# Performance work log

Hardware: AMD Instinct MI355X
Metric: run time of the kernel (lower is better)

Reference implementation:

```python
import jax, jax.numpy as jnp
import numpy as np


def _graph_conv_mean(x, src, dst, edge_weight, W_rel, W_root, b, num_nodes):
    # messages: gather source features, optionally scale by edge weight
    msg = x[src]  # [E, D]
    if edge_weight is not None:
        msg = msg * edge_weight[:, None]
    # mean aggregation over incoming edges per destination node
    summed = jax.ops.segment_sum(msg, dst, num_segments=num_nodes)  # [N, D]
    count = jax.ops.segment_sum(jnp.ones((src.shape[0],), x.dtype), dst, num_segments=num_nodes)
    mean = summed / jnp.maximum(count, 1.0)[:, None]
    # out = lin_rel(mean) + lin_root(x) + bias
    return mean @ W_rel + x @ W_root + b


def setup_inputs() -> dict:
    key = jax.random.key(0)
    ks = jax.random.split(key, 8)
    N, E, D, H, C = 100000, 1600000, 128, 32, 5
    x = jax.random.normal(ks[0], (N, D), dtype=jnp.float32)
    edge_index = jax.random.randint(ks[1], (2, E), 0, N, dtype=jnp.int64)
    edge_weight = jax.random.uniform(ks[2], (E,), dtype=jnp.float32)
    W_rel1 = jax.random.normal(ks[3], (D, H), dtype=jnp.float32) / np.sqrt(D)
    W_root1 = jax.random.normal(ks[4], (D, H), dtype=jnp.float32) / np.sqrt(D)
    b1 = jnp.zeros((H,), jnp.float32)
    W_rel2 = jax.random.normal(ks[5], (H, C), dtype=jnp.float32) / np.sqrt(H)
    W_root2 = jax.random.normal(ks[6], (H, C), dtype=jnp.float32) / np.sqrt(H)
    b2 = jnp.zeros((C,), jnp.float32)
    return {"x": x, "edge_index": edge_index, "edge_weight": edge_weight,
            "W_rel1": W_rel1, "W_root1": W_root1, "b1": b1,
            "W_rel2": W_rel2, "W_root2": W_root2, "b2": b2}


def reference(x, edge_index, edge_weight, W_rel1, W_root1, b1, W_rel2, W_root2, b2):
    N = x.shape[0]
    src, dst = edge_index[0], edge_index[1]
    # conv1 with edge_weight
    h = _graph_conv_mean(x, src, dst, edge_weight, W_rel1, W_root1, b1, N)
    h = jax.nn.relu(h)
    # dropout is identity at inference (training=False)
    # conv2 without edge_weight
    out = _graph_conv_mean(h, src, dst, None, W_rel2, W_root2, b2, N)
    return jax.nn.log_softmax(out, axis=1)
```

## Files before the change

kernel.cpp:

```cpp
#include <hip/hip_runtime.h>
#include <math.h>

#define N_NODES 100000
#define E_EDGES 1600000
#define D_IN    128
#define H_MID   32
#define C_OUT   5

#define BSHIFT 8
#define BNODES 256
#define NBKT   391
#define BCAP   4800
#define SRC_BITS 17
#define SRC_MASK 0x1FFFF

#define KP 136

typedef __attribute__((ext_vector_type(8))) short bf16x8;
typedef __attribute__((ext_vector_type(4))) float f32x4;

__device__ inline unsigned f2bf(float f) {
    unsigned u = __float_as_uint(f);
    return (u + 0x7FFFu + ((u >> 16) & 1u)) >> 16;
}

__global__ void k_prep(const float* __restrict__ Wrel,
                       const float* __restrict__ Wroot,
                       int* __restrict__ bucket_cursor,
                       unsigned short* __restrict__ wt_g) {
    int tid = threadIdx.x;
    bucket_cursor[tid] = 0;
    for (int i = tid; i < 64 * 128; i += 512) {
        int n = i >> 7, k = i & 127;
        float v = (n < H_MID) ? Wrel[k * H_MID + n] : Wroot[k * H_MID + (n - H_MID)];
        wt_g[i] = (unsigned short)f2bf(v);
    }
}

__global__ __launch_bounds__(256) void k1_mfma(
    const float* __restrict__ x,
    const unsigned short* __restrict__ wt_g,
    const float* __restrict__ b1,
    unsigned short* __restrict__ xrelh,
    float* __restrict__ xroot) {
    __shared__ unsigned short xs[64 * KP];
    int tid = threadIdx.x;
    int nodeBase = blockIdx.x * 64;

    #pragma unroll
    for (int it = 0; it < 16; ++it) {
        int idx = it * 256 + tid;
        int row = idx >> 6, kp = idx & 63;
        int node = nodeBase + row;
        float2 v = make_float2(0.f, 0.f);
        if (node < N_NODES)
            v = *(const float2*)(x + (size_t)node * D_IN + kp * 2);
        unsigned pk = f2bf(v.x) | (f2bf(v.y) << 16);
        *(unsigned*)(xs + row * KP + kp * 2) = pk;
    }
    __syncthreads();

    int lane = tid & 63;
    int wv = tid >> 6;
    int m = lane & 15;
    int quad = lane >> 4;

    f32x4 acc[4];
    #pragma unroll
    for (int nt = 0; nt < 4; ++nt) acc[nt] = (f32x4){0.f, 0.f, 0.f, 0.f};

    #pragma unroll
    for (int kk = 0; kk < 4; ++kk) {
        int k0 = kk * 32 + quad * 8;
        bf16x8 a = *(const bf16x8*)(xs + (wv * 16 + m) * KP + k0);
        #pragma unroll
        for (int nt = 0; nt < 4; ++nt) {
            bf16x8 b = *(const bf16x8*)(wt_g + (nt * 16 + m) * 128 + k0);
            acc[nt] = __builtin_amdgcn_mfma_f32_16x16x32_bf16(a, b, acc[nt], 0, 0, 0);
        }
    }

    #pragma unroll
    for (int nt = 0; nt < 4; ++nt) {
        #pragma unroll
        for (int r = 0; r < 4; ++r) {
            int node = nodeBase + wv * 16 + quad * 4 + r;
            int colg = nt * 16 + m;
            if (node < N_NODES) {
                if (colg < H_MID) {
                    xrelh[(size_t)node * H_MID + colg] =
                        (unsigned short)f2bf(acc[nt][r]);
                } else {
                    int c = colg - H_MID;
                    xroot[(size_t)node * H_MID + c] = acc[nt][r] + b1[c];
                }
            }
        }
    }
}

__global__ __launch_bounds__(1024) void k_binA(
    const int* __restrict__ src,
    const int* __restrict__ dst,
    const float* __restrict__ ew,
    int* __restrict__ bucket_cursor,
    int2* __restrict__ staged) {
    __shared__ int cnt[NBKT];
    __shared__ int lstart[NBKT];
    __shared__ int gbase[NBKT];
    __shared__ int scanbuf[512];
    __shared__ int2 ebuf[2048];
    __shared__ short bbuf[2048];
    int tid = threadIdx.x;
    int eBase = blockIdx.x * 2048;

    if (tid < NBKT) cnt[tid] = 0;
    __syncthreads();

    int b[2], rank[2], packed[2], wbits[2];
    bool valid[2];
    #pragma unroll
    for (int u = 0; u < 2; ++u) {
        int e = eBase + u * 1024 + tid;
        valid[u] = (e < E_EDGES);
        b[u] = 0; rank[u] = 0; packed[u] = 0; wbits[u] = 0;
        if (valid[u]) {
            int d = dst[e];
            int s = src[e];
            wbits[u] = __float_as_int(ew[e]);
            b[u] = d >> BSHIFT;
            packed[u] = ((d & (BNODES - 1)) << SRC_BITS) | s;
            rank[u] = atomicAdd(&cnt[b[u]], 1);
        }
    }
    __syncthreads();

    if (tid < 512) scanbuf[tid] = (tid < NBKT) ? cnt[tid] : 0;
    __syncthreads();
    for (int off = 1; off < 512; off <<= 1) {
        int t = 0;
        if (tid < 512 && tid >= off) t = scanbuf[tid - off];
        __syncthreads();
        if (tid < 512) scanbuf[tid] += t;
        __syncthreads();
    }
    if (tid < NBKT) {
        lstart[tid] = scanbuf[tid] - cnt[tid];
        gbase[tid]  = atomicAdd(&bucket_cursor[tid], cnt[tid]);
    }
    __syncthreads();
    int total = scanbuf[NBKT - 1];

    #pragma unroll
    for (int u = 0; u < 2; ++u) {
        if (valid[u]) {
            int slot = lstart[b[u]] + rank[u];
            ebuf[slot] = make_int2(packed[u], wbits[u]);
            bbuf[slot] = (short)b[u];
        }
    }
    __syncthreads();

    for (int t = tid; t < total; t += 1024) {
        int2 ev = ebuf[t];
        int bb = bbuf[t];
        int gpos = gbase[bb] + (t - lstart[bb]);
        if (gpos < BCAP)
            staged[(size_t)bb * BCAP + gpos] = ev;
    }
}

__global__ __launch_bounds__(1024) void k_binB2(
    const int* __restrict__ bucket_cursor,
    const int2* __restrict__ staged,
    int* __restrict__ deg,
    int* __restrict__ offsets,
    int* __restrict__ csr_src,
    int* __restrict__ csr_wi) {
    __shared__ int hist[BNODES];
    __shared__ int scanb[BNODES];
    __shared__ int cur[BNODES];
    __shared__ int sbase[512];
    int tid = threadIdx.x;
    int b = blockIdx.x;

    if (tid < 512) {
        int c = (tid < NBKT) ? bucket_cursor[tid] : 0;
        sbase[tid] = (c > BCAP) ? BCAP : c;
    }
    if (tid < BNODES) hist[tid] = 0;
    __syncthreads();
    for (int off = 1; off < 512; off <<= 1) {
        int t = 0;
        if (tid < 512 && tid >= off) t = sbase[tid - off];
        __syncthreads();
        if (tid < 512) sbase[tid] += t;
        __syncthreads();
    }
    int count = bucket_cursor[b];
    if (count > BCAP) count = BCAP;
    int base = sbase[b] - count;
    int nodeBase = b << BSHIFT;
    const int2* sp = staged + (size_t)b * BCAP;

    for (int i = tid; i < count; i += 1024)
        atomicAdd(&hist[((unsigned)sp[i].x) >> SRC_BITS], 1);
    __syncthreads();

    int v = 0;
    if (tid < BNODES) {
        v = hist[tid];
        scanb[tid] = v;
    }
    __syncthreads();
    for (int off = 1; off < BNODES; off <<= 1) {
        int t = 0;
        if (tid < BNODES && tid >= off) t = scanb[tid - off];
        __syncthreads();
        if (tid < BNODES) scanb[tid] += t;
        __syncthreads();
    }
    if (tid < BNODES) {
        int excl = scanb[tid] - v;
        int node = nodeBase + tid;
        if (node < N_NODES) {
            deg[node]     = v;
            offsets[node] = base + excl;
        }
        cur[tid] = excl;
    }
    __syncthreads();

    for (int i = tid; i < count; i += 1024) {
        int2 ev = sp[i];
        int local = ((unsigned)ev.x) >> SRC_BITS;
        int pos = base + atomicAdd(&cur[local], 1);
        csr_src[pos] = ev.x & SRC_MASK;
        csr_wi[pos]  = ev.y;
    }
}

__global__ __launch_bounds__(256) void k_layer1(
    const int* __restrict__ offsets,
    const int* __restrict__ deg,
    const int* __restrict__ csr_src,
    const float* __restrict__ csr_w,
    const unsigned short* __restrict__ xrelh,
    const float* __restrict__ xroot,
    const float* __restrict__ Wrel2,
    const float* __restrict__ Wroot2,
    const float* __restrict__ b2,
    float* __restrict__ h2rel,
    float* __restrict__ h2root) {
    int node = blockIdx.x * 16 + (threadIdx.x >> 4);
    int lane = threadIdx.x & 15;
    int beg = offsets[node];
    int dg  = deg[node];
    int end = beg + dg;

    float acc0 = 0.f, acc1 = 0.f;
    int i = beg;
    int nfull = dg >> 3;
    if (nfull) {
        int s[8]; float w[8];
        #pragma unroll
        for (int u = 0; u < 8; ++u) { s[u] = csr_src[i + u]; w[u] = csr_w[i + u]; }
        for (int bb = 1; bb < nfull; ++bb) {
            unsigned v[8];
            #pragma unroll
            for (int u = 0; u < 8; ++u)
                v[u] = *(const unsigned*)(xrelh + (size_t)s[u] * H_MID + lane * 2);
            int s2[8]; float w2[8];
            #pragma unroll
            for (int u = 0; u < 8; ++u) { s2[u] = csr_src[i + 8 + u]; w2[u] = csr_w[i + 8 + u]; }
            #pragma unroll
            for (int u = 0; u < 8; ++u) {
                acc0 += __uint_as_float((v[u] & 0xFFFFu) << 16) * w[u];
                acc1 += __uint_as_float(v[u] & 0xFFFF0000u) * w[u];
            }
            #pragma unroll
            for (int u = 0; u < 8; ++u) { s[u] = s2[u]; w[u] = w2[u]; }
            i += 8;
        }
        unsigned v[8];
        #pragma unroll
        for (int u = 0; u < 8; ++u)
            v[u] = *(const unsigned*)(xrelh + (size_t)s[u] * H_MID + lane * 2);
        #pragma unroll
        for (int u = 0; u < 8; ++u) {
            acc0 += __uint_as_float((v[u] & 0xFFFFu) << 16) * w[u];
            acc1 += __uint_as_float(v[u] & 0xFFFF0000u) * w[u];
        }
        i += 8;
    }
    for (; i < end; ++i) {
        int s0 = csr_src[i];
        float w0 = csr_w[i];
        unsigned v0 = *(const unsigned*)(xrelh + (size_t)s0 * H_MID + lane * 2);
        acc0 += __uint_as_float((v0 & 0xFFFFu) << 16) * w0;
        acc1 += __uint_as_float(v0 & 0xFFFF0000u) * w0;
    }

    float inv = 1.0f / fmaxf((float)dg, 1.0f);
    float2 rt = *(const float2*)(xroot + (size_t)node * H_MID + lane * 2);
    float h0 = fmaxf(acc0 * inv + rt.x, 0.f);
    float h1 = fmaxf(acc1 * inv + rt.y, 0.f);

    float p[2 * C_OUT];
    #pragma unroll
    for (int j = 0; j < C_OUT; ++j) {
        p[j]         = h0 * Wrel2[(2 * lane) * C_OUT + j]
                     + h1 * Wrel2[(2 * lane + 1) * C_OUT + j];
        p[C_OUT + j] = h0 * Wroot2[(2 * lane) * C_OUT + j]
                     + h1 * Wroot2[(2 * lane + 1) * C_OUT + j];
    }
    #pragma unroll
    for (int mm = 8; mm > 0; mm >>= 1) {
        #pragma unroll
        for (int j = 0; j < 2 * C_OUT; ++j)
            p[j] += __shfl_xor(p[j], mm, 16);
    }
    if (lane == 0) {
        #pragma unroll
        for (int j = 0; j < C_OUT; ++j) {
            h2rel[(size_t)node * C_OUT + j]  = p[j];
            h2root[(size_t)node * C_OUT + j] = p[C_OUT + j] + b2[j];
        }
    }
}

__global__ __launch_bounds__(256) void k_layer2(
    const int* __restrict__ offsets,
    const int* __restrict__ deg,
    const int* __restrict__ csr_src,
    const float* __restrict__ h2rel,
    const float* __restrict__ h2root,
    float* __restrict__ out) {
    int node = blockIdx.x * 32 + (threadIdx.x >> 3);
    int lane = threadIdx.x & 7;
    int beg = offsets[node];
    int dg  = deg[node];
    int end = beg + dg;

    float acc = 0.f;
    if (lane < C_OUT) {
        int i = beg;
        int nfull = dg >> 3;
        if (nfull) {
            int s[8];
            #pragma unroll
            for (int u = 0; u < 8; ++u) s[u] = csr_src[i + u];
            for (int bb = 1; bb < nfull; ++bb) {
                float v[8];
                #pragma unroll
                for (int u = 0; u < 8; ++u)
                    v[u] = h2rel[(size_t)s[u] * C_OUT + lane];
                int s2[8];
                #pragma unroll
                for (int u = 0; u < 8; ++u) s2[u] = csr_src[i + 8 + u];
                #pragma unroll
                for (int u = 0; u < 8; ++u) acc += v[u];
                #pragma unroll
                for (int u = 0; u < 8; ++u) s[u] = s2[u];
                i += 8;
            }
            #pragma unroll
            for (int u = 0; u < 8; ++u)
                acc += h2rel[(size_t)s[u] * C_OUT + lane];
            i += 8;
        }
        for (; i < end; ++i)
            acc += h2rel[(size_t)csr_src[i] * C_OUT + lane];
    }
    float inv = 1.0f / fmaxf((float)dg, 1.0f);
    float o = (lane < C_OUT)
                  ? acc * inv + h2root[(size_t)node * C_OUT + lane]
                  : -INFINITY;
    float m = o;
    #pragma unroll
    for (int dd = 4; dd > 0; dd >>= 1) m = fmaxf(m, __shfl_xor(m, dd, 8));
    float e = (lane < C_OUT) ? expf(o - m) : 0.f;
    float ssum = e;
    #pragma unroll
    for (int dd = 4; dd > 0; dd >>= 1) ssum += __shfl_xor(ssum, dd, 8);
    float lse = m + logf(ssum);
    if (lane < C_OUT)
        out[(size_t)node * C_OUT + lane] = o - lse;
}

extern "C" void kernel_launch(void* const* d_in, const int* in_sizes, int n_in,
                              void* d_out, int out_size, void* d_ws, size_t ws_size,
                              hipStream_t stream) {
    const float* x      = (const float*)d_in[0];
    const int*   ei     = (const int*)d_in[1];
    const float* ew     = (const float*)d_in[2];
    const float* Wrel1  = (const float*)d_in[3];
    const float* Wroot1 = (const float*)d_in[4];
    const float* b1     = (const float*)d_in[5];
    const float* Wrel2  = (const float*)d_in[6];
    const float* Wroot2 = (const float*)d_in[7];
    const float* b2     = (const float*)d_in[8];
    float* out = (float*)d_out;

    const int* src = ei;
    const int* dst = ei + E_EDGES;

    char* ws = (char*)d_ws;
    int*   deg           = (int*)ws;
    int*   bucket_cursor = deg + N_NODES;
    unsigned short* wt_g = (unsigned short*)(bucket_cursor + 512);
    int*   offsets       = (int*)(wt_g + 64 * 128);
    int*   csr_src       = offsets + N_NODES;
    int*   csr_wi        = csr_src + E_EDGES;
    unsigned short* xrelh = (unsigned short*)(csr_wi + E_EDGES);
    float* xroot         = (float*)(xrelh + (size_t)N_NODES * H_MID);
    float* h2rel         = xroot + (size_t)N_NODES * H_MID;
    float* h2root        = h2rel + (size_t)N_NODES * C_OUT;
    int2*  staged        = (int2*)xrelh;

    k_prep<<<1, 512, 0, stream>>>(Wrel1, Wroot1, bucket_cursor, wt_g);

    k_binA<<<(E_EDGES + 2047) / 2048, 1024, 0, stream>>>(src, dst, ew,
                                                         bucket_cursor, staged);
    k_binB2<<<NBKT, 1024, 0, stream>>>(bucket_cursor, staged,
                                       deg, offsets, csr_src, csr_wi);

    k1_mfma<<<(N_NODES + 63) / 64, 256, 0, stream>>>(x, wt_g, b1,
                                                     xrelh, xroot);

    k_layer1<<<N_NODES / 16, 256, 0, stream>>>(offsets, deg, csr_src,
                                               (const float*)csr_wi,
                                               xrelh, xroot, Wrel2, Wroot2, b2,
                                               h2rel, h2root);

    k_layer2<<<N_NODES / 32, 256, 0, stream>>>(offsets, deg, csr_src,
                                               h2rel, h2root, out);
}
```

Measured before the change: 227.1 us.

## Replace two-pass bucketed CSR build with global atomic count-scan-scatter

Drops the bucketed two-pass binning (local shared-memory sort into a staged buffer, then per-bucket histogram and scatter). CSR is now built by a global atomic degree count, a single-block scan over all nodes, and an atomic scatter of src and weight into CSR positions. This removes the staging buffer, the bucket capacity limit and the heavy shared-memory kernels. The cost is many scattered global atomics with poor locality, a serial single-block scan, and an extra kernel launch. Neighbor order within each node becomes nondeterministic.

```diff
diff --git a/kernel.cpp b/kernel.cpp
--- a/kernel.cpp
+++ b/kernel.cpp
@@ -7,13 +7,6 @@
 #define H_MID   32
 #define C_OUT   5
 
-#define BSHIFT 8
-#define BNODES 256
-#define NBKT   391
-#define BCAP   4800
-#define SRC_BITS 17
-#define SRC_MASK 0x1FFFF
-
 #define KP 136
 
 typedef __attribute__((ext_vector_type(8))) short bf16x8;
@@ -24,16 +17,82 @@
     return (u + 0x7FFFu + ((u >> 16) & 1u)) >> 16;
 }
 
-__global__ void k_prep(const float* __restrict__ Wrel,
-                       const float* __restrict__ Wroot,
-                       int* __restrict__ bucket_cursor,
-                       unsigned short* __restrict__ wt_g) {
+__global__ __launch_bounds__(1024) void k_prep(
+    const float* __restrict__ Wrel,
+    const float* __restrict__ Wroot,
+    int* __restrict__ deg,
+    unsigned short* __restrict__ wt_g) {
+    int gid = blockIdx.x * 1024 + threadIdx.x;
+    if (gid < N_NODES) deg[gid] = 0;
+    if (blockIdx.x == 0) {
+        for (int i = threadIdx.x; i < 64 * 128; i += 1024) {
+            int n = i >> 7, k = i & 127;
+            float v = (n < H_MID) ? Wrel[k * H_MID + n]
+                                  : Wroot[k * H_MID + (n - H_MID)];
+            wt_g[i] = (unsigned short)f2bf(v);
+        }
+    }
+}
+
+__global__ __launch_bounds__(256) void k_deg(
+    const int* __restrict__ dst,
+    int* __restrict__ deg) {
+    int e0 = blockIdx.x * 1024 + threadIdx.x;
+    #pragma unroll
+    for (int u = 0; u < 4; ++u) {
+        int e = e0 + u * 256;
+        if (e < E_EDGES) atomicAdd(&deg[dst[e]], 1);
+    }
+}
+
+__global__ __launch_bounds__(1024) void k_scan(
+    const int* __restrict__ deg,
+    int* __restrict__ offsets,
+    int* __restrict__ cur) {
+    __shared__ int tsum[1024];
     int tid = threadIdx.x;
-    bucket_cursor[tid] = 0;
-    for (int i = tid; i < 64 * 128; i += 512) {
-        int n = i >> 7, k = i & 127;
-        float v = (n < H_MID) ? Wrel[k * H_MID + n] : Wroot[k * H_MID + (n - H_MID)];
-        wt_g[i] = (unsigned short)f2bf(v);
+    int base = tid * 98;
+    int s = 0;
+    for (int i = 0; i < 98; ++i) {
+        int n = base + i;
+        if (n < N_NODES) s += deg[n];
+    }
+    tsum[tid] = s;
+    __syncthreads();
+    for (int off = 1; off < 1024; off <<= 1) {
+        int t = (tid >= off) ? tsum[tid - off] : 0;
+        __syncthreads();
+        tsum[tid] += t;
+        __syncthreads();
+    }
+    int run = (tid > 0) ? tsum[tid - 1] : 0;
+    for (int i = 0; i < 98; ++i) {
+        int n = base + i;
+        if (n < N_NODES) {
+            offsets[n] = run;
+            cur[n] = run;
+            run += deg[n];
+        }
+    }
+}
+
+__global__ __launch_bounds__(256) void k_scatter(
+    const int* __restrict__ src,
+    const int* __restrict__ dst,
+    const float* __restrict__ ew,
+    int* __restrict__ cur,
+    int* __restrict__ csr_src,
+    int* __restrict__ csr_wi) {
+    int e0 = blockIdx.x * 1024 + threadIdx.x;
+    #pragma unroll
+    for (int u = 0; u < 4; ++u) {
+        int e = e0 + u * 256;
+        if (e < E_EDGES) {
+            int d = dst[e];
+            int pos = atomicAdd(&cur[d], 1);
+            csr_src[pos] = src[e];
+            csr_wi[pos]  = __float_as_int(ew[e]);
+        }
     }
 }
 
@@ -96,147 +155,6 @@
                 }
             }
         }
-    }
-}
-
-__global__ __launch_bounds__(1024) void k_binA(
-    const int* __restrict__ src,
-    const int* __restrict__ dst,
-    const float* __restrict__ ew,
-    int* __restrict__ bucket_cursor,
-    int2* __restrict__ staged) {
-    __shared__ int cnt[NBKT];
-    __shared__ int lstart[NBKT];
-    __shared__ int gbase[NBKT];
-    __shared__ int scanbuf[512];
-    __shared__ int2 ebuf[2048];
-    __shared__ short bbuf[2048];
-    int tid = threadIdx.x;
-    int eBase = blockIdx.x * 2048;
-
-    if (tid < NBKT) cnt[tid] = 0;
-    __syncthreads();
-
-    int b[2], rank[2], packed[2], wbits[2];
-    bool valid[2];
-    #pragma unroll
-    for (int u = 0; u < 2; ++u) {
-        int e = eBase + u * 1024 + tid;
-        valid[u] = (e < E_EDGES);
-        b[u] = 0; rank[u] = 0; packed[u] = 0; wbits[u] = 0;
-        if (valid[u]) {
-            int d = dst[e];
-            int s = src[e];
-            wbits[u] = __float_as_int(ew[e]);
-            b[u] = d >> BSHIFT;
-            packed[u] = ((d & (BNODES - 1)) << SRC_BITS) | s;
-            rank[u] = atomicAdd(&cnt[b[u]], 1);
-        }
-    }
-    __syncthreads();
-
-    if (tid < 512) scanbuf[tid] = (tid < NBKT) ? cnt[tid] : 0;
-    __syncthreads();
-    for (int off = 1; off < 512; off <<= 1) {
-        int t = 0;
-        if (tid < 512 && tid >= off) t = scanbuf[tid - off];
-        __syncthreads();
-        if (tid < 512) scanbuf[tid] += t;
-        __syncthreads();
-    }
-    if (tid < NBKT) {
-        lstart[tid] = scanbuf[tid] - cnt[tid];
-        gbase[tid]  = atomicAdd(&bucket_cursor[tid], cnt[tid]);
-    }
-    __syncthreads();
-    int total = scanbuf[NBKT - 1];
-
-    #pragma unroll
-    for (int u = 0; u < 2; ++u) {
-        if (valid[u]) {
-            int slot = lstart[b[u]] + rank[u];
-            ebuf[slot] = make_int2(packed[u], wbits[u]);
-            bbuf[slot] = (short)b[u];
-        }
-    }
-    __syncthreads();
-
-    for (int t = tid; t < total; t += 1024) {
-        int2 ev = ebuf[t];
-        int bb = bbuf[t];
-        int gpos = gbase[bb] + (t - lstart[bb]);
-        if (gpos < BCAP)
-            staged[(size_t)bb * BCAP + gpos] = ev;
-    }
-}
-
-__global__ __launch_bounds__(1024) void k_binB2(
-    const int* __restrict__ bucket_cursor,
-    const int2* __restrict__ staged,
-    int* __restrict__ deg,
-    int* __restrict__ offsets,
-    int* __restrict__ csr_src,
-    int* __restrict__ csr_wi) {
-    __shared__ int hist[BNODES];
-    __shared__ int scanb[BNODES];
-    __shared__ int cur[BNODES];
-    __shared__ int sbase[512];
-    int tid = threadIdx.x;
-    int b = blockIdx.x;
-
-    if (tid < 512) {
-        int c = (tid < NBKT) ? bucket_cursor[tid] : 0;
-        sbase[tid] = (c > BCAP) ? BCAP : c;
-    }
-    if (tid < BNODES) hist[tid] = 0;
-    __syncthreads();
-    for (int off = 1; off < 512; off <<= 1) {
-        int t = 0;
-        if (tid < 512 && tid >= off) t = sbase[tid - off];
-        __syncthreads();
-        if (tid < 512) sbase[tid] += t;
-        __syncthreads();
-    }
-    int count = bucket_cursor[b];
-    if (count > BCAP) count = BCAP;
-    int base = sbase[b] - count;
-    int nodeBase = b << BSHIFT;
-    const int2* sp = staged + (size_t)b * BCAP;
-
-    for (int i = tid; i < count; i += 1024)
-        atomicAdd(&hist[((unsigned)sp[i].x) >> SRC_BITS], 1);
-    __syncthreads();
-
-    int v = 0;
-    if (tid < BNODES) {
-        v = hist[tid];
-        scanb[tid] = v;
-    }
-    __syncthreads();
-    for (int off = 1; off < BNODES; off <<= 1) {
-        int t = 0;
-        if (tid < BNODES && tid >= off) t = scanb[tid - off];
-        __syncthreads();
-        if (tid < BNODES) scanb[tid] += t;
-        __syncthreads();
-    }
-    if (tid < BNODES) {
-        int excl = scanb[tid] - v;
-        int node = nodeBase + tid;
-        if (node < N_NODES) {
-            deg[node]     = v;
-            offsets[node] = base + excl;
-        }
-        cur[tid] = excl;
-    }
-    __syncthreads();
-
-    for (int i = tid; i < count; i += 1024) {
-        int2 ev = sp[i];
-        int local = ((unsigned)ev.x) >> SRC_BITS;
-        int pos = base + atomicAdd(&cur[local], 1);
-        csr_src[pos] = ev.x & SRC_MASK;
-        csr_wi[pos]  = ev.y;
     }
 }
 
@@ -407,23 +325,23 @@
 
     char* ws = (char*)d_ws;
     int*   deg           = (int*)ws;
-    int*   bucket_cursor = deg + N_NODES;
-    unsigned short* wt_g = (unsigned short*)(bucket_cursor + 512);
-    int*   offsets       = (int*)(wt_g + 64 * 128);
-    int*   csr_src       = offsets + N_NODES;
+    int*   offsets       = deg + N_NODES;
+    int*   cur           = offsets + N_NODES;
+    int*   csr_src       = cur + N_NODES;
     int*   csr_wi        = csr_src + E_EDGES;
-    unsigned short* xrelh = (unsigned short*)(csr_wi + E_EDGES);
+    unsigned short* wt_g = (unsigned short*)(csr_wi + E_EDGES);
+    unsigned short* xrelh = wt_g + 64 * 128;
     float* xroot         = (float*)(xrelh + (size_t)N_NODES * H_MID);
     float* h2rel         = xroot + (size_t)N_NODES * H_MID;
     float* h2root        = h2rel + (size_t)N_NODES * C_OUT;
-    int2*  staged        = (int2*)xrelh;
-
-    k_prep<<<1, 512, 0, stream>>>(Wrel1, Wroot1, bucket_cursor, wt_g);
-
-    k_binA<<<(E_EDGES + 2047) / 2048, 1024, 0, stream>>>(src, dst, ew,
-                                                         bucket_cursor, staged);
-    k_binB2<<<NBKT, 1024, 0, stream>>>(bucket_cursor, staged,
-                                       deg, offsets, csr_src, csr_wi);
+
+    k_prep<<<(N_NODES + 1023) / 1024, 1024, 0, stream>>>(Wrel1, Wroot1,
+                                                         deg, wt_g);
+
+    k_deg<<<(E_EDGES + 1023) / 1024, 256, 0, stream>>>(dst, deg);
+    k_scan<<<1, 1024, 0, stream>>>(deg, offsets, cur);
+    k_scatter<<<(E_EDGES + 1023) / 1024, 256, 0, stream>>>(src, dst, ew, cur,
+                                                           csr_src, csr_wi);
 
     k1_mfma<<<(N_NODES + 63) / 64, 256, 0, stream>>>(x, wt_g, b1,
                                                      xrelh, xroot);
```

New measurement: 608.1 us. 2.68x slower.
